# Optimization experiments

Measured on AMD Instinct MI355X. Metric: run time of the kernel, lower is better.

## Reference

```python
import jax, jax.numpy as jnp
import numpy as np

B, N = 4, 4096
CIN, COUT = 64, 64
K, R, BOX = 3, 32, 4
MLP = COUT * 4
HEADS = 4
EPS = 0.0


def setup_inputs() -> dict:
    key = jax.random.key(0)
    ks = jax.random.split(key, 16)
    s = lambda i, shape: jax.random.normal(ks[i], shape, jnp.float32) * 0.05
    return dict(
        features=jax.random.normal(ks[0], (B, CIN, N), jnp.float32),
        coords=jax.random.normal(ks[1], (B, 3, N), jnp.float32),
        conv_w=s(2, (COUT, CIN, K, K, K)), conv_b=jnp.zeros((COUT,), jnp.float32),
        ln1_g=jnp.ones((COUT,), jnp.float32), ln1_b=jnp.zeros((COUT,), jnp.float32),
        qkv_w=s(3, (3 * COUT, COUT)), qkv_b=jnp.zeros((3 * COUT,), jnp.float32),
        proj_w=s(4, (COUT, COUT)), proj_b=jnp.zeros((COUT,), jnp.float32),
        ln2_g=jnp.ones((COUT,), jnp.float32), ln2_b=jnp.zeros((COUT,), jnp.float32),
        mlp_w1=s(5, (MLP, COUT)), mlp_b1=jnp.zeros((MLP,), jnp.float32),
        mlp_w2=s(6, (COUT, MLP)), mlp_b2=jnp.zeros((COUT,), jnp.float32),
        se_w1=s(7, (COUT // 8, COUT)), se_w2=s(8, (COUT, COUT // 8)),
        pt_in_w=s(9, (COUT, CIN)), pt_in_b=jnp.zeros((COUT,), jnp.float32),
        q_w=s(10, (COUT // 4, COUT)), k_w=s(11, (COUT // 4, COUT)),
        v_w=s(12, (COUT, COUT)),
        trans_w=s(13, (COUT, COUT)), trans_b=jnp.zeros((COUT,), jnp.float32),
    )


def layernorm(x, g, b):
    m = x.mean(-1, keepdims=True)
    v = x.var(-1, keepdims=True)
    return (x - m) * jax.lax.rsqrt(v + 1e-5) * g + b


def voxelize(features, coords):
    # PVCNN-style: center, normalize to [0,1], scale to [0, R-1]; scatter-mean.
    c = coords - coords.mean(axis=2, keepdims=True)  # (B,3,N)
    mx = jnp.sqrt((c ** 2).sum(axis=1, keepdims=True)).max(axis=2, keepdims=True)
    nc = c / (2.0 * mx + EPS) + 0.5
    nc = jnp.clip(nc * R, 0.0, R - 1)  # float coords in [0, R-1]
    vc = jnp.round(nc).astype(jnp.int32)
    idx = (vc[:, 0] * R + vc[:, 1]) * R + vc[:, 2]
    idx = (idx + jnp.arange(B, dtype=jnp.int32)[:, None] * R ** 3).reshape(-1)
    flat = features.transpose(0, 2, 1).reshape(B * N, CIN)
    sums = jax.ops.segment_sum(flat, idx, num_segments=B * R ** 3)
    cnt = jax.ops.segment_sum(jnp.ones((B * N,), jnp.float32), idx, num_segments=B * R ** 3)
    avg = sums / jnp.maximum(cnt, 1.0)[:, None]
    grid = avg.reshape(B, R, R, R, CIN).transpose(0, 4, 1, 2, 3)  # (B,C,R,R,R)
    return grid, nc


def devoxelize(grid, nc):
    # trilinear gather from (B,C,R,R,R) at float coords nc (B,3,N)
    g = grid.reshape(B, COUT, R ** 3)
    x0 = jnp.floor(nc)
    f = nc - x0
    x0 = x0.astype(jnp.int32)
    out = jnp.zeros((B, COUT, N), jnp.float32)
    for dx in (0, 1):
        for dy in (0, 1):
            for dz in (0, 1):
                xi = jnp.clip(x0[:, 0] + dx, 0, R - 1)
                yi = jnp.clip(x0[:, 1] + dy, 0, R - 1)
                zi = jnp.clip(x0[:, 2] + dz, 0, R - 1)
                idx = (xi * R + yi) * R + zi  # (B,N)
                w = ((f[:, 0] if dx else 1 - f[:, 0]) *
                     (f[:, 1] if dy else 1 - f[:, 1]) *
                     (f[:, 2] if dz else 1 - f[:, 2]))
                vals = jnp.take_along_axis(g, jnp.broadcast_to(idx[:, None, :], (B, COUT, N)), axis=2)
                out = out + vals * w[:, None, :]
    return out


def voxel_encoder(grid, conv_w, conv_b, ln1_g, ln1_b, qkv_w, qkv_b, proj_w, proj_b,
                  ln2_g, ln2_b, mlp_w1, mlp_b1, mlp_w2, mlp_b2):
    x = jax.lax.conv_general_dilated(grid, conv_w, (1, 1, 1), 'SAME',
                                     dimension_numbers=('NCDHW', 'OIDHW', 'NCDHW'))
    x = jax.nn.relu(x + conv_b[None, :, None, None, None])
    nb = R // BOX
    # window partition -> (B*nb^3, BOX^3, C)
    t = x.transpose(0, 2, 3, 4, 1).reshape(B, nb, BOX, nb, BOX, nb, BOX, COUT)
    t = t.transpose(0, 1, 3, 5, 2, 4, 6, 7).reshape(B * nb ** 3, BOX ** 3, COUT)
    h = layernorm(t, ln1_g, ln1_b)
    qkv = h @ qkv_w.T + qkv_b
    q, k, v = jnp.split(qkv, 3, axis=-1)
    hd = COUT // HEADS
    sh = lambda z: z.reshape(z.shape[0], z.shape[1], HEADS, hd).transpose(0, 2, 1, 3)
    q, k, v = sh(q), sh(k), sh(v)
    attn = jax.nn.softmax(jnp.einsum('whid,whjd->whij', q, k) / np.float32(np.sqrt(hd)), axis=-1)
    o = jnp.einsum('whij,whjd->whid', attn, v).transpose(0, 2, 1, 3).reshape(t.shape)
    t = t + (o @ proj_w.T + proj_b)
    h = layernorm(t, ln2_g, ln2_b)
    t = t + (jax.nn.gelu(h @ mlp_w1.T + mlp_b1) @ mlp_w2.T + mlp_b2)
    t = t.reshape(B, nb, nb, nb, BOX, BOX, BOX, COUT)
    t = t.transpose(0, 1, 4, 2, 5, 3, 6, 7).reshape(B, R, R, R, COUT)
    return t.transpose(0, 4, 1, 2, 3)


def se3d(x, w1, w2):
    s = x.mean(axis=(2, 3, 4))  # (B,C)
    s = jax.nn.sigmoid(jax.nn.relu(s @ w1.T) @ w2.T)
    return x * s[:, :, None, None, None]


def point_branch(features, pt_in_w, pt_in_b, q_w, k_w, v_w, trans_w, trans_b):
    # PCT-style offset self-attention over points (shared transformer)
    x = jax.nn.relu(jnp.einsum('oc,bcn->bon', pt_in_w, features) + pt_in_b[None, :, None])
    q = jnp.einsum('dc,bcn->bdn', q_w, x)
    k = jnp.einsum('dc,bcn->bdn', k_w, x)
    v = jnp.einsum('oc,bcn->bon', v_w, x)
    attn = jax.nn.softmax(jnp.einsum('bdn,bdm->bnm', q, k) / np.float32(np.sqrt(q.shape[1])), axis=-1)
    o = jnp.einsum('bom,bnm->bon', v, attn)
    off = jax.nn.relu(jnp.einsum('oc,bcn->bon', trans_w, x - o) + trans_b[None, :, None])
    return x + off


def reference(features, coords, conv_w, conv_b, ln1_g, ln1_b, qkv_w, qkv_b, proj_w, proj_b,
              ln2_g, ln2_b, mlp_w1, mlp_b1, mlp_w2, mlp_b2, se_w1, se_w2,
              pt_in_w, pt_in_b, q_w, k_w, v_w, trans_w, trans_b):
    grid, nc = voxelize(features, coords)
    vf = voxel_encoder(grid, conv_w, conv_b, ln1_g, ln1_b, qkv_w, qkv_b, proj_w, proj_b,
                       ln2_g, ln2_b, mlp_w1, mlp_b1, mlp_w2, mlp_b2)
    vf = se3d(vf, se_w1, se_w2)
    vf = devoxelize(vf, nc)
    fused = vf + point_branch(features, pt_in_w, pt_in_b, q_w, k_w, v_w, trans_w, trans_b)
    return fused, coords
```

## Files before the change

kernel.cpp:

```cpp
#include <hip/hip_runtime.h>

#define BN 4
#define NP 4096
#define RV 32
#define VX (RV*RV*RV)

typedef __attribute__((ext_vector_type(8))) short bf16x8;
typedef __attribute__((ext_vector_type(4))) float f32x4;

__device__ __forceinline__ float bf2f(unsigned short u){
  union{unsigned u;float f;}v; v.u=((unsigned)u)<<16; return v.f; }
__device__ __forceinline__ unsigned short f2bf(float f){
  union{float f;unsigned u;}v; v.f=f; unsigned r=v.u + 0x7fffu + ((v.u>>16)&1u);
  return (unsigned short)(r>>16); }
__device__ __forceinline__ float2 bfp2f2(unsigned p){
  union{unsigned u;float f;}a,b; a.u=p<<16; b.u=p&0xffff0000u;
  float2 r; r.x=a.f; r.y=b.f; return r; }
__device__ __forceinline__ unsigned pack2bf(float a, float b){
  return (unsigned)f2bf(a) | ((unsigned)f2bf(b) << 16); }

union ABu { uint4 u; bf16x8 v; };

__global__ void stats_kernel(const float* __restrict__ coords, float* __restrict__ stats)
{
  __shared__ float red[256];
  __shared__ float mean[3];
  const int b = blockIdx.x;
  const int tid = threadIdx.x;
  float s0=0.f,s1=0.f,s2=0.f;
  for (int n = tid; n < NP; n += 256) {
    s0 += coords[((size_t)(b*3)+0)*NP + n];
    s1 += coords[((size_t)(b*3)+1)*NP + n];
    s2 += coords[((size_t)(b*3)+2)*NP + n];
  }
  float sv[3] = {s0,s1,s2};
  for (int ax = 0; ax < 3; ax++) {
    __syncthreads();
    red[tid] = sv[ax];
    __syncthreads();
    for (int st = 128; st > 0; st >>= 1) {
      if (tid < st) red[tid] += red[tid + st];
      __syncthreads();
    }
    if (tid == 0) mean[ax] = red[0] * (1.f / NP);
  }
  __syncthreads();
  float mx = 0.f;
  for (int n = tid; n < NP; n += 256) {
    float d0 = coords[((size_t)(b*3)+0)*NP + n] - mean[0];
    float d1 = coords[((size_t)(b*3)+1)*NP + n] - mean[1];
    float d2 = coords[((size_t)(b*3)+2)*NP + n] - mean[2];
    mx = fmaxf(mx, sqrtf(d0*d0 + d1*d1 + d2*d2));
  }
  __syncthreads();
  red[tid] = mx;
  __syncthreads();
  for (int st = 128; st > 0; st >>= 1) {
    if (tid < st) red[tid] = fmaxf(red[tid], red[tid + st]);
    __syncthreads();
  }
  if (tid == 0) {
    stats[b*4+0] = mean[0]; stats[b*4+1] = mean[1];
    stats[b*4+2] = mean[2]; stats[b*4+3] = red[0];
  }
}

__global__ __launch_bounds__(256) void scatter_kernel(
    const float* __restrict__ features, const float* __restrict__ coords,
    const float* __restrict__ stats, float* __restrict__ nc,
    float* __restrict__ sums, float* __restrict__ cnt)
{
  __shared__ float f_s[64*65];
  const int tid = threadIdx.x;
  const int blk = blockIdx.x;
  const int b = blk >> 6;
  const int n0 = (blk & 63) * 64;
  for (int e = tid; e < 4096; e += 256) {
    int c = e >> 6, nl = e & 63;
    f_s[nl*65 + c] = features[((size_t)(b*64 + c))*NP + n0 + nl];
  }
  const int part = tid & 3, nl = tid >> 2;
  const int n = n0 + nl;
  float m0 = stats[b*4+0], m1 = stats[b*4+1], m2 = stats[b*4+2], mx = stats[b*4+3];
  float inv = 1.f / (2.f * mx);
  float c0 = (coords[((size_t)(b*3)+0)*NP + n] - m0) * inv + 0.5f;
  float c1 = (coords[((size_t)(b*3)+1)*NP + n] - m1) * inv + 0.5f;
  float c2 = (coords[((size_t)(b*3)+2)*NP + n] - m2) * inv + 0.5f;
  float g0 = fminf(fmaxf(c0 * 32.f, 0.f), 31.f);
  float g1 = fminf(fmaxf(c1 * 32.f, 0.f), 31.f);
  float g2 = fminf(fmaxf(c2 * 32.f, 0.f), 31.f);
  int v0 = (int)rintf(g0), v1 = (int)rintf(g1), v2 = (int)rintf(g2);
  int idx = (v0*32 + v1)*32 + v2 + b*VX;
  if (part == 0) {
    nc[((size_t)(b*3)+0)*NP + n] = g0;
    nc[((size_t)(b*3)+1)*NP + n] = g1;
    nc[((size_t)(b*3)+2)*NP + n] = g2;
    atomicAdd(&cnt[idx], 1.f);
  }
  __syncthreads();
  float* sp = sums + (size_t)idx*64;
  #pragma unroll
  for (int j = 0; j < 16; j++) {
    int i = part*16 + j;
    atomicAdd(&sp[i], f_s[nl*65 + i]);
  }
}

__global__ void wprep_kernel(const float* __restrict__ wt, unsigned short* __restrict__ wpre)
{
  int t = blockIdx.x*256 + threadIdx.x;
  if (t >= 27*64*8) return;
  int c16 = t & 7, o = (t >> 3) & 63, tap = t >> 9;
  size_t dst = ((size_t)(tap*64 + o)*8 + (c16 ^ (o & 7))) * 8;
  #pragma unroll
  for (int j = 0; j < 8; j++) {
    int i = c16*8 + j;
    wpre[dst + j] = f2bf(wt[(o*64 + i)*27 + tap]);
  }
}

__global__ void eprep_kernel(const float* __restrict__ qkv_w, const float* __restrict__ proj_w,
                             const float* __restrict__ w1, const float* __restrict__ w2,
                             const float* __restrict__ pt_in_w, const float* __restrict__ q_w,
                             const float* __restrict__ k_w, const float* __restrict__ v_w,
                             unsigned short* __restrict__ dst)
{
  int t = blockIdx.x*256 + threadIdx.x;
  if (t >= 59392) return;
  float v;
  if (t < 4096)       v = qkv_w[t] * 0.25f;
  else if (t < 12288) v = qkv_w[t];
  else if (t < 16384) v = proj_w[t-12288];
  else if (t < 32768) v = w1[t-16384];
  else if (t < 49152) v = w2[t-32768];
  else {
    int t2 = t - 49152;
    if (t2 < 4096)      v = pt_in_w[t2];
    else if (t2 < 5120) v = q_w[t2-4096] * 0.25f;
    else if (t2 < 6144) v = k_w[t2-5120];
    else                v = v_w[t2-6144];
  }
  dst[t] = f2bf(v);
}

__global__ __launch_bounds__(256) void conv_mfma_kernel(
    const float* __restrict__ sums, const float* __restrict__ cnt,
    const unsigned short* __restrict__ wpre,
    const float* __restrict__ bias, unsigned short* __restrict__ gout)
{
  __shared__ uint4 plane[6*34*8];
  __shared__ uint4 wsm[3*64*8];
  const int tid = threadIdx.x;
  const int blk = blockIdx.x;
  const int yq = blk & 7, z = (blk >> 3) & 31, b = blk >> 8;
  const int y0 = yq * 4;
  const int w  = tid >> 6;
  const int lm = tid & 15;
  const int kg = (tid >> 4) & 3;

  f32x4 acc[2][4];
  #pragma unroll
  for (int mt = 0; mt < 2; mt++)
    #pragma unroll
    for (int nt = 0; nt < 4; nt++)
      #pragma unroll
      for (int r = 0; r < 4; r++) acc[mt][nt][r] = 0.f;

  float bv[4];
  #pragma unroll
  for (int nt = 0; nt < 4; nt++) bv[nt] = bias[nt*16 + lm];

  for (int kd = 0; kd < 3; kd++) {
    const int zz = z + kd - 1;
    if (zz < 0 || zz >= 32) continue;
    __syncthreads();
    for (int e = tid; e < 6*34*8; e += 256) {
      int c16 = e & 7;
      int sx  = (e >> 3) % 34;
      int yl  = e / (34*8);
      int yy = y0 - 1 + yl, x = sx - 1;
      uint4 val = make_uint4(0u,0u,0u,0u);
      if (yy >= 0 && yy < 32 && x >= 0 && x < 32) {
        size_t vox = (size_t)(b*VX) + (zz*32 + yy)*32 + x;
        float rc = 1.f / fmaxf(cnt[vox], 1.f);
        const float* src = sums + vox*64 + c16*8;
        float4 f0 = *(const float4*)(src);
        float4 f1 = *(const float4*)(src + 4);
        val.x = pack2bf(f0.x*rc, f0.y*rc);
        val.y = pack2bf(f0.z*rc, f0.w*rc);
        val.z = pack2bf(f1.x*rc, f1.y*rc);
        val.w = pack2bf(f1.z*rc, f1.w*rc);
      }
      plane[(yl*34 + sx)*8 + (c16 ^ (sx & 7))] = val;
    }
    for (int kh = 0; kh < 3; kh++) {
      __syncthreads();
      const uint4* wsrc = (const uint4*)wpre + (size_t)((kd*3 + kh)*3)*512;
      for (int e = tid; e < 1536; e += 256) wsm[e] = wsrc[e];
      __syncthreads();
      const int yi = w + kh;
      #pragma unroll
      for (int kw = 0; kw < 3; kw++) {
        const int sxa = lm + kw, sxb = sxa + 16;
        const int swz = sxa & 7;
        #pragma unroll
        for (int ch = 0; ch < 2; ch++) {
          const int cb = ch*4 + kg;
          ABu a0, a1, w0, w1, w2, w3;
          a0.u = plane[(yi*34 + sxa)*8 + (cb ^ swz)];
          a1.u = plane[(yi*34 + sxb)*8 + (cb ^ swz)];
          const int wsz = cb ^ (lm & 7);
          w0.u = wsm[(kw*64 +      lm)*8 + wsz];
          w1.u = wsm[(kw*64 + 16 + lm)*8 + wsz];
          w2.u = wsm[(kw*64 + 32 + lm)*8 + wsz];
          w3.u = wsm[(kw*64 + 48 + lm)*8 + wsz];
          acc[0][0] = __builtin_amdgcn_mfma_f32_16x16x32_bf16(a0.v, w0.v, acc[0][0], 0,0,0);
          acc[1][0] = __builtin_amdgcn_mfma_f32_16x16x32_bf16(a1.v, w0.v, acc[1][0], 0,0,0);
          acc[0][1] = __builtin_amdgcn_mfma_f32_16x16x32_bf16(a0.v, w1.v, acc[0][1], 0,0,0);
          acc[1][1] = __builtin_amdgcn_mfma_f32_16x16x32_bf16(a1.v, w1.v, acc[1][1], 0,0,0);
          acc[0][2] = __builtin_amdgcn_mfma_f32_16x16x32_bf16(a0.v, w2.v, acc[0][2], 0,0,0);
          acc[1][2] = __builtin_amdgcn_mfma_f32_16x16x32_bf16(a1.v, w2.v, acc[1][2], 0,0,0);
          acc[0][3] = __builtin_amdgcn_mfma_f32_16x16x32_bf16(a0.v, w3.v, acc[0][3], 0,0,0);
          acc[1][3] = __builtin_amdgcn_mfma_f32_16x16x32_bf16(a1.v, w3.v, acc[1][3], 0,0,0);
        }
      }
    }
  }
  const int y = y0 + w;
  #pragma unroll
  for (int mt = 0; mt < 2; mt++) {
    #pragma unroll
    for (int r = 0; r < 4; r++) {
      const int x = mt*16 + kg*4 + r;
      unsigned short* dst = gout + ((size_t)(b*VX) + (z*32 + y)*32 + x)*64 + lm;
      #pragma unroll
      for (int nt = 0; nt < 4; nt++)
        dst[nt*16] = f2bf(fmaxf(acc[mt][nt][r] + bv[nt], 0.f));
    }
  }
}

__global__ __launch_bounds__(256) void encoder_kernel(
    unsigned short* __restrict__ grid,
    const float* __restrict__ ln1_g, const float* __restrict__ ln1_b,
    const float* __restrict__ qkv_b, const float* __restrict__ proj_b,
    const float* __restrict__ ln2_g, const float* __restrict__ ln2_b,
    const float* __restrict__ b1, const float* __restrict__ b2,
    const unsigned short* __restrict__ encw,
    float* __restrict__ se_sum)
{
  __shared__ unsigned short t_b[64*72];
  __shared__ unsigned short h_b[64*72];
  __shared__ unsigned short q_b[64*72];
  __shared__ unsigned short k_b[64*72];
  __shared__ unsigned short v_b[64*72];
  __shared__ float mean_s[64], rstd_s[64];
  __shared__ float sered[256];

  const unsigned short* wqb = encw;
  const unsigned short* wpb = encw + 12288;
  const unsigned short* w1b = encw + 16384;
  const unsigned short* w2b = encw + 32768;

  const int tid = threadIdx.x;
  const int w = tid >> 6;
  const int lane = tid & 63;
  const int cl = lane & 15;
  const int quad = lane >> 4;
  const int win = blockIdx.x;
  const int b = win >> 9, wn = win & 511;
  const int zb = wn >> 6, yb = (wn >> 3) & 7, xb = wn & 7;
  const size_t gb = (size_t)b * VX * 64;

  for (int e = tid; e < 1024; e += 256) {
    int tok = e >> 4, cg = e & 15;
    int zl = tok >> 4, yl = (tok >> 2) & 3, xl = tok & 3;
    int vox = ((zb*4+zl)*32 + (yb*4+yl))*32 + (xb*4+xl);
    *(uint2*)(t_b + tok*72 + cg*4) = *(const uint2*)(grid + gb + (size_t)vox*64 + cg*4);
  }
  __syncthreads();
  {
    int i = tid >> 2, part = tid & 3;
    float sum = 0.f, sq = 0.f;
    for (int c = part; c < 64; c += 4) { float x = bf2f(t_b[i*72+c]); sum += x; sq += x*x; }
    sum += __shfl_xor(sum, 1); sq += __shfl_xor(sq, 1);
    sum += __shfl_xor(sum, 2); sq += __shfl_xor(sq, 2);
    if (part == 0) {
      float m = sum * (1.f/64.f);
      float var = sq * (1.f/64.f) - m*m;
      mean_s[i] = m; rstd_s[i] = rsqrtf(var + 1e-5f);
    }
  }
  __syncthreads();
  for (int e = tid; e < 4096; e += 256) {
    int tok = e >> 6, c = e & 63;
    float h = (bf2f(t_b[tok*72+c]) - mean_s[tok]) * rstd_s[tok] * ln1_g[c] + ln1_b[c];
    h_b[tok*72 + c] = f2bf(h);
  }
  __syncthreads();
  {
    #pragma unroll
    for (int ci = 0; ci < 3; ci++) {
      const int d0 = 48*w + ci*16;
      ABu a0, a1;
      a0.u = *(const uint4*)(wqb + (d0 + cl)*64 + quad*8);
      a1.u = *(const uint4*)(wqb + (d0 + cl)*64 + 32 + quad*8);
      float4 bias4 = *(const float4*)(qkv_b + d0 + quad*4);
      if (d0 < 64) { bias4.x *= 0.25f; bias4.y *= 0.25f; bias4.z *= 0.25f; bias4.w *= 0.25f; }
      #pragma unroll
      for (int tt = 0; tt < 4; tt++) {
        ABu h0, h1;
        h0.u = *(const uint4*)(h_b + (tt*16 + cl)*72 + quad*8);
        h1.u = *(const uint4*)(h_b + (tt*16 + cl)*72 + 32 + quad*8);
        f32x4 d = {0.f,0.f,0.f,0.f};
        d = __builtin_amdgcn_mfma_f32_16x16x32_bf16(a0.v, h0.v, d, 0,0,0);
        d = __builtin_amdgcn_mfma_f32_16x16x32_bf16(a1.v, h1.v, d, 0,0,0);
        if (d0 < 64) {
          *(uint2*)(q_b + (tt*16+cl)*72 + d0 + quad*4) =
            make_uint2(pack2bf(d[0]+bias4.x, d[1]+bias4.y),
                       pack2bf(d[2]+bias4.z, d[3]+bias4.w));
        } else if (d0 < 128) {
          *(uint2*)(k_b + (tt*16+cl)*72 + (d0-64) + quad*4) =
            make_uint2(pack2bf(d[0]+bias4.x, d[1]+bias4.y),
                       pack2bf(d[2]+bias4.z, d[3]+bias4.w));
        } else {
          const float* bp = (const float*)&bias4;
          #pragma unroll
          for (int r = 0; r < 4; r++)
            v_b[((d0-128) + quad*4 + r)*72 + tt*16 + cl] = f2bf(d[r] + bp[r]);
        }
      }
    }
  }
  __syncthreads();
  uint2 pk[4];
  {
    const uint4 z4 = make_uint4(0u,0u,0u,0u);
    #pragma unroll
    for (int h = 0; h < 4; h++) {
      const int hb = h*16;
      ABu bq;
      if (quad < 2) bq.u = *(const uint4*)(q_b + (w*16 + cl)*72 + hb + quad*8);
      else bq.u = z4;
      float sc[4][4];
      #pragma unroll
      for (int tj = 0; tj < 4; tj++) {
        ABu ak;
        if (quad < 2) ak.u = *(const uint4*)(k_b + (tj*16 + cl)*72 + hb + quad*8);
        else ak.u = z4;
        f32x4 d = {0.f,0.f,0.f,0.f};
        d = __builtin_amdgcn_mfma_f32_16x16x32_bf16(ak.v, bq.v, d, 0,0,0);
        #pragma unroll
        for (int r = 0; r < 4; r++) sc[tj][r] = d[r];
      }
      float mx = -1e30f;
      #pragma unroll
      for (int tj = 0; tj < 4; tj++)
        #pragma unroll
        for (int r = 0; r < 4; r++) mx = fmaxf(mx, sc[tj][r]);
      mx = fmaxf(mx, __shfl_xor(mx, 16));
      mx = fmaxf(mx, __shfl_xor(mx, 32));
      float psum = 0.f;
      #pragma unroll
      for (int tj = 0; tj < 4; tj++) {
        float p0 = __expf(sc[tj][0]-mx), p1 = __expf(sc[tj][1]-mx);
        float p2 = __expf(sc[tj][2]-mx), p3 = __expf(sc[tj][3]-mx);
        psum += p0+p1+p2+p3;
        *(uint2*)(h_b + (w*16+cl)*72 + tj*16 + quad*4) =
            make_uint2(pack2bf(p0,p1), pack2bf(p2,p3));
      }
      psum += __shfl_xor(psum, 16);
      psum += __shfl_xor(psum, 32);
      float inv = 1.f / psum;
      f32x4 oacc = {0.f,0.f,0.f,0.f};
      #pragma unroll
      for (int kk = 0; kk < 2; kk++) {
        ABu av, bp;
        av.u = *(const uint4*)(v_b + (hb + cl)*72 + kk*32 + quad*8);
        bp.u = *(const uint4*)(h_b + (w*16 + cl)*72 + kk*32 + quad*8);
        oacc = __builtin_amdgcn_mfma_f32_16x16x32_bf16(av.v, bp.v, oacc, 0,0,0);
      }
      pk[h] = make_uint2(pack2bf(oacc[0]*inv, oacc[1]*inv),
                         pack2bf(oacc[2]*inv, oacc[3]*inv));
    }
  }
  __syncthreads();
  #pragma unroll
  for (int h = 0; h < 4; h++)
    *(uint2*)(k_b + (w*16+cl)*72 + h*16 + quad*4) = pk[h];
  __syncthreads();
  {
    const int c0 = w*16;
    ABu a0, a1;
    a0.u = *(const uint4*)(wpb + (c0 + cl)*64 + quad*8);
    a1.u = *(const uint4*)(wpb + (c0 + cl)*64 + 32 + quad*8);
    float4 pb4 = *(const float4*)(proj_b + c0 + quad*4);
    #pragma unroll
    for (int tt = 0; tt < 4; tt++) {
      ABu o0, o1;
      o0.u = *(const uint4*)(k_b + (tt*16 + cl)*72 + quad*8);
      o1.u = *(const uint4*)(k_b + (tt*16 + cl)*72 + 32 + quad*8);
      f32x4 d = {0.f,0.f,0.f,0.f};
      d = __builtin_amdgcn_mfma_f32_16x16x32_bf16(a0.v, o0.v, d, 0,0,0);
      d = __builtin_amdgcn_mfma_f32_16x16x32_bf16(a1.v, o1.v, d, 0,0,0);
      uint2* tp = (uint2*)(t_b + (tt*16+cl)*72 + c0 + quad*4);
      uint2 told = *tp;
      float2 t01 = bfp2f2(told.x), t23 = bfp2f2(told.y);
      *tp = make_uint2(pack2bf(t01.x + d[0] + pb4.x, t01.y + d[1] + pb4.y),
                       pack2bf(t23.x + d[2] + pb4.z, t23.y + d[3] + pb4.w));
    }
  }
  __syncthreads();
  {
    int i = tid >> 2, part = tid & 3;
    float sum = 0.f, sq = 0.f;
    for (int c = part; c < 64; c += 4) { float x = bf2f(t_b[i*72+c]); sum += x; sq += x*x; }
    sum += __shfl_xor(sum, 1); sq += __shfl_xor(sq, 1);
    sum += __shfl_xor(sum, 2); sq += __shfl_xor(sq, 2);
    if (part == 0) {
      float m = sum * (1.f/64.f);
      float var = sq * (1.f/64.f) - m*m;
      mean_s[i] = m; rstd_s[i] = rsqrtf(var + 1e-5f);
    }
  }
  __syncthreads();
  for (int e = tid; e < 4096; e += 256) {
    int tok = e >> 6, c = e & 63;
    float h = (bf2f(t_b[tok*72+c]) - mean_s[tok]) * rstd_s[tok] * ln2_g[c] + ln2_b[c];
    h_b[tok*72 + c] = f2bf(h);
  }
  __syncthreads();
  {
    const int c0 = w*16;
    ABu hb0[4], hb1[4];
    #pragma unroll
    for (int tt = 0; tt < 4; tt++) {
      hb0[tt].u = *(const uint4*)(h_b + (tt*16 + cl)*72 + quad*8);
      hb1[tt].u = *(const uint4*)(h_b + (tt*16 + cl)*72 + 32 + quad*8);
    }
    f32x4 acc2[4];
    #pragma unroll
    for (int tt = 0; tt < 4; tt++)
      #pragma unroll
      for (int r = 0; r < 4; r++) acc2[tt][r] = 0.f;
    for (int ch = 0; ch < 4; ch++) {
      const int m0 = ch*64 + w*16;
      ABu a0, a1;
      a0.u = *(const uint4*)(w1b + (m0 + cl)*64 + quad*8);
      a1.u = *(const uint4*)(w1b + (m0 + cl)*64 + 32 + quad*8);
      float4 b14 = *(const float4*)(b1 + m0 + quad*4);
      const float* bp = (const float*)&b14;
      #pragma unroll
      for (int tt = 0; tt < 4; tt++) {
        f32x4 d = {0.f,0.f,0.f,0.f};
        d = __builtin_amdgcn_mfma_f32_16x16x32_bf16(a0.v, hb0[tt].v, d, 0,0,0);
        d = __builtin_amdgcn_mfma_f32_16x16x32_bf16(a1.v, hb1[tt].v, d, 0,0,0);
        float g[4];
        #pragma unroll
        for (int r = 0; r < 4; r++) {
          float x = d[r] + bp[r];
          float u = 1.5957691f * (x + 0.044715f*x*x*x);
          g[r] = x / (1.f + __expf(-u));
        }
        *(uint2*)(q_b + (tt*16+cl)*72 + w*16 + quad*4) =
            make_uint2(pack2bf(g[0],g[1]), pack2bf(g[2],g[3]));
      }
      __syncthreads();
      ABu a20, a21;
      a20.u = *(const uint4*)(w2b + (c0 + cl)*256 + ch*64 + quad*8);
      a21.u = *(const uint4*)(w2b + (c0 + cl)*256 + ch*64 + 32 + quad*8);
      #pragma unroll
      for (int tt = 0; tt < 4; tt++) {
        ABu bh0, bh1;
        bh0.u = *(const uint4*)(q_b + (tt*16 + cl)*72 + quad*8);
        bh1.u = *(const uint4*)(q_b + (tt*16 + cl)*72 + 32 + quad*8);
        acc2[tt] = __builtin_amdgcn_mfma_f32_16x16x32_bf16(a20.v, bh0.v, acc2[tt], 0,0,0);
        acc2[tt] = __builtin_amdgcn_mfma_f32_16x16x32_bf16(a21.v, bh1.v, acc2[tt], 0,0,0);
      }
      __syncthreads();
    }
    float4 b24 = *(const float4*)(b2 + c0 + quad*4);
    #pragma unroll
    for (int tt = 0; tt < 4; tt++) {
      uint2* tp = (uint2*)(t_b + (tt*16+cl)*72 + c0 + quad*4);
      uint2 told = *tp;
      float2 t01 = bfp2f2(told.x), t23 = bfp2f2(told.y);
      *tp = make_uint2(pack2bf(t01.x + acc2[tt][0] + b24.x, t01.y + acc2[tt][1] + b24.y),
                       pack2bf(t23.x + acc2[tt][2] + b24.z, t23.y + acc2[tt][3] + b24.w));
    }
  }
  __syncthreads();
  for (int e = tid; e < 1024; e += 256) {
    int tok = e >> 4, cg = e & 15;
    int zl = tok >> 4, yl = (tok >> 2) & 3, xl = tok & 3;
    int vox = ((zb*4+zl)*32 + (yb*4+yl))*32 + (xb*4+xl);
    *(uint2*)(grid + gb + (size_t)vox*64 + cg*4) = *(const uint2*)(t_b + tok*72 + cg*4);
  }
  {
    int c = tid & 63, quarter = tid >> 6;
    float ps = 0.f;
    #pragma unroll
    for (int t = 0; t < 16; t++) ps += bf2f(t_b[(quarter*16+t)*72 + c]);
    sered[quarter*64 + c] = ps;
  }
  __syncthreads();
  if (tid < 64)
    atomicAdd(&se_sum[b*64 + tid],
              sered[tid] + sered[64+tid] + sered[128+tid] + sered[192+tid]);
}

__global__ void se_kernel(const float* __restrict__ se_sum, const float* __restrict__ w1,
                          const float* __restrict__ w2, float* __restrict__ scale)
{
  __shared__ float mean_s[256];
  __shared__ float z1[32];
  int tid = threadIdx.x;
  mean_s[tid] = se_sum[tid] * (1.f / VX);
  __syncthreads();
  if (tid < 32) {
    int bb = tid >> 3, j = tid & 7;
    float a = 0.f;
    for (int c = 0; c < 64; c++) a += mean_s[bb*64 + c] * w1[j*64 + c];
    z1[tid] = fmaxf(a, 0.f);
  }
  __syncthreads();
  int b = tid >> 6, c = tid & 63;
  float a = 0.f;
  for (int j = 0; j < 8; j++) a += z1[b*8 + j] * w2[c*8 + j];
  scale[tid] = 1.f / (1.f + __expf(-a));
}

__global__ __launch_bounds__(256) void point_in_kernel(
    const float* __restrict__ features, const float* __restrict__ pt_in_b,
    const unsigned short* __restrict__ ptw,
    float* __restrict__ x_t, unsigned short* __restrict__ q_bf,
    unsigned short* __restrict__ k_bf, unsigned short* __restrict__ v_tt)
{
  __shared__ unsigned short f_b[64*72];
  __shared__ unsigned short x_b[64*72];
  const int tid = threadIdx.x;
  const int blk = blockIdx.x;
  const int b = blk >> 6;
  const int n0 = (blk & 63) * 64;
  const int w = tid >> 6;
  const int lane = tid & 63;
  const int cl = lane & 15;
  const int quad = lane >> 4;

  for (int e = tid; e < 4096; e += 256) {
    int c = e >> 6, nl = e & 63;
    f_b[nl*72 + c] = f2bf(features[((size_t)(b*64 + c))*NP + n0 + nl]);
  }
  __syncthreads();
  const int m0 = w*16;
  {
    ABu a0, a1;
    a0.u = *(const uint4*)(ptw + (m0 + cl)*64 + quad*8);
    a1.u = *(const uint4*)(ptw + (m0 + cl)*64 + 32 + quad*8);
    float4 bi = *(const float4*)(pt_in_b + m0 + quad*4);
    #pragma unroll
    for (int tt = 0; tt < 4; tt++) {
      ABu f0, f1;
      f0.u = *(const uint4*)(f_b + (tt*16 + cl)*72 + quad*8);
      f1.u = *(const uint4*)(f_b + (tt*16 + cl)*72 + 32 + quad*8);
      f32x4 d = {0.f,0.f,0.f,0.f};
      d = __builtin_amdgcn_mfma_f32_16x16x32_bf16(a0.v, f0.v, d, 0,0,0);
      d = __builtin_amdgcn_mfma_f32_16x16x32_bf16(a1.v, f1.v, d, 0,0,0);
      float x0 = fmaxf(d[0]+bi.x, 0.f), x1 = fmaxf(d[1]+bi.y, 0.f);
      float x2 = fmaxf(d[2]+bi.z, 0.f), x3 = fmaxf(d[3]+bi.w, 0.f);
      const int n = tt*16 + cl;
      *(float4*)&x_t[((size_t)(b*NP) + n0 + n)*64 + m0 + quad*4] =
          make_float4(x0, x1, x2, x3);
      *(uint2*)(x_b + n*72 + m0 + quad*4) = make_uint2(pack2bf(x0,x1), pack2bf(x2,x3));
    }
  }
  __syncthreads();
  {
    const unsigned short* vwb = ptw + 6144;
    ABu a0, a1;
    a0.u = *(const uint4*)(vwb + (m0 + cl)*64 + quad*8);
    a1.u = *(const uint4*)(vwb + (m0 + cl)*64 + 32 + quad*8);
    #pragma unroll
    for (int tt = 0; tt < 4; tt++) {
      ABu x0, x1;
      x0.u = *(const uint4*)(x_b + (tt*16 + cl)*72 + quad*8);
      x1.u = *(const uint4*)(x_b + (tt*16 + cl)*72 + 32 + quad*8);
      f32x4 d = {0.f,0.f,0.f,0.f};
      d = __builtin_amdgcn_mfma_f32_16x16x32_bf16(a0.v, x0.v, d, 0,0,0);
      d = __builtin_amdgcn_mfma_f32_16x16x32_bf16(a1.v, x1.v, d, 0,0,0);
      const int n = n0 + tt*16 + cl;
      #pragma unroll
      for (int r = 0; r < 4; r++)
        v_tt[((size_t)(b*64) + m0 + quad*4 + r)*NP + n] = f2bf(d[r]);
    }
  }
  {
    const int which = w & 1, half = w >> 1;
    const unsigned short* wp = ptw + (which ? 5120 : 4096);
    unsigned short* dst = which ? k_bf : q_bf;
    ABu a0, a1;
    a0.u = *(const uint4*)(wp + cl*64 + quad*8);
    a1.u = *(const uint4*)(wp + cl*64 + 32 + quad*8);
    #pragma unroll
    for (int th = 0; th < 2; th++) {
      const int tt = half*2 + th;
      ABu x0, x1;
      x0.u = *(const uint4*)(x_b + (tt*16 + cl)*72 + quad*8);
      x1.u = *(const uint4*)(x_b + (tt*16 + cl)*72 + 32 + quad*8);
      f32x4 d = {0.f,0.f,0.f,0.f};
      d = __builtin_amdgcn_mfma_f32_16x16x32_bf16(a0.v, x0.v, d, 0,0,0);
      d = __builtin_amdgcn_mfma_f32_16x16x32_bf16(a1.v, x1.v, d, 0,0,0);
      const int n = tt*16 + cl;
      *(uint2*)(dst + ((size_t)(b*NP) + n0 + n)*16 + quad*4) =
          make_uint2(pack2bf(d[0],d[1]), pack2bf(d[2],d[3]));
    }
  }
}

__global__ __launch_bounds__(256) void point_attn_kernel(
    const unsigned short* __restrict__ q_bf, const unsigned short* __restrict__ k_bf,
    const unsigned short* __restrict__ v_tt,
    float* __restrict__ opart, float2* __restrict__ mlbuf)
{
  __shared__ unsigned short q_s[64*24];
  __shared__ unsigned short k_sh[2][64*24];
  __shared__ unsigned short v_sh[2][64*72];
  __shared__ unsigned short p_s[64*72];
  const int tid = threadIdx.x;
  const int blk = blockIdx.x;
  const int b = blk >> 8;
  const int nb = (blk >> 2) & 63;
  const int s = blk & 3;
  const int n0 = nb * 64;
  const int t_beg = s*16, t_end = s*16 + 16;
  const int w = tid >> 6;
  const int lane = tid & 63;
  const int cl = lane & 15;
  const int quad = lane >> 4;
  const uint4 z4 = make_uint4(0u,0u,0u,0u);

  const unsigned* qbu = (const unsigned*)q_bf;
  const unsigned* kbu = (const unsigned*)k_bf;
  const unsigned* vtu = (const unsigned*)v_tt;
  unsigned* q_su = (unsigned*)q_s;

  {
    unsigned* kd = (unsigned*)k_sh[0];
    unsigned* vd = (unsigned*)v_sh[0];
    for (int e = tid; e < 512; e += 256) {
      int tok = e >> 3, du = e & 7;
      q_su[tok*12 + du] = qbu[((size_t)(b*NP) + n0 + tok)*8 + du];
      kd[tok*12 + du]   = kbu[((size_t)(b*NP) + t_beg*64 + tok)*8 + du];
    }
    for (int e = tid; e < 2048; e += 256) {
      int cc = e >> 5, tu = e & 31;
      vd[cc*36 + tu] = vtu[((size_t)(b*64) + cc)*2048 + t_beg*32 + tu];
    }
  }
  float m_run = -1e30f, l_run = 0.f;
  f32x4 acc[4];
  #pragma unroll
  for (int ct = 0; ct < 4; ct++)
    #pragma unroll
    for (int r = 0; r < 4; r++) acc[ct][r] = 0.f;
  __syncthreads();

  ABu bq;
  if (quad < 2) bq.u = *(const uint4*)(q_s + (w*16 + cl)*24 + quad*8);
  else bq.u = z4;

  for (int t = t_beg; t < t_end; t++) {
    const int cur = t & 1;
    unsigned pk[2], pv[8];
    if (t+1 < t_end) {
      const int m1 = (t+1)*64;
      #pragma unroll
      for (int i = 0; i < 2; i++) {
        int e = tid + i*256;
        pk[i] = kbu[((size_t)(b*NP) + m1 + (e>>3))*8 + (e&7)];
      }
      #pragma unroll
      for (int i = 0; i < 8; i++) {
        int e = tid + i*256;
        pv[i] = vtu[((size_t)(b*64) + (e>>5))*2048 + (m1>>1) + (e&31)];
      }
    }
    const unsigned short* ks = k_sh[cur];
    const unsigned short* vs = v_sh[cur];
    float sc[4][4];
    #pragma unroll
    for (int tj = 0; tj < 4; tj++) {
      ABu ak;
      if (quad < 2) ak.u = *(const uint4*)(ks + (tj*16 + cl)*24 + quad*8);
      else ak.u = z4;
      f32x4 d = {0.f,0.f,0.f,0.f};
      d = __builtin_amdgcn_mfma_f32_16x16x32_bf16(ak.v, bq.v, d, 0,0,0);
      #pragma unroll
      for (int r = 0; r < 4; r++) sc[tj][r] = d[r];
    }
    float tmax = -1e30f;
    #pragma unroll
    for (int tj = 0; tj < 4; tj++)
      #pragma unroll
      for (int r = 0; r < 4; r++) tmax = fmaxf(tmax, sc[tj][r]);
    tmax = fmaxf(tmax, __shfl_xor(tmax, 16));
    tmax = fmaxf(tmax, __shfl_xor(tmax, 32));
    float mnew = fmaxf(m_run, tmax);
    float alpha = __expf(m_run - mnew);
    float psum = 0.f;
    #pragma unroll
    for (int tj = 0; tj < 4; tj++) {
      float p0 = __expf(sc[tj][0]-mnew), p1 = __expf(sc[tj][1]-mnew);
      float p2 = __expf(sc[tj][2]-mnew), p3 = __expf(sc[tj][3]-mnew);
      psum += p0+p1+p2+p3;
      *(uint2*)(p_s + (w*16+cl)*72 + tj*16 + quad*4) =
          make_uint2(pack2bf(p0,p1), pack2bf(p2,p3));
    }
    psum += __shfl_xor(psum, 16);
    psum += __shfl_xor(psum, 32);
    l_run = l_run*alpha + psum;
    m_run = mnew;
    #pragma unroll
    for (int ct = 0; ct < 4; ct++)
      #pragma unroll
      for (int r = 0; r < 4; r++) acc[ct][r] *= alpha;
    #pragma unroll
    for (int kk = 0; kk < 2; kk++) {
      ABu bp;
      bp.u = *(const uint4*)(p_s + (w*16 + cl)*72 + kk*32 + quad*8);
      #pragma unroll
      for (int ct = 0; ct < 4; ct++) {
        ABu av;
        av.u = *(const uint4*)(vs + (ct*16 + cl)*72 + kk*32 + quad*8);
        acc[ct] = __builtin_amdgcn_mfma_f32_16x16x32_bf16(av.v, bp.v, acc[ct], 0,0,0);
      }
    }
    __syncthreads();
    if (t+1 < t_end) {
      unsigned* kd = (unsigned*)k_sh[1-cur];
      unsigned* vd = (unsigned*)v_sh[1-cur];
      #pragma unroll
      for (int i = 0; i < 2; i++) {
        int e = tid + i*256;
        kd[(e>>3)*12 + (e&7)] = pk[i];
      }
      #pragma unroll
      for (int i = 0; i < 8; i++) {
        int e = tid + i*256;
        vd[(e>>5)*36 + (e&31)] = pv[i];
      }
    }
    __syncthreads();
  }
  const int tok = n0 + w*16 + cl;
  #pragma unroll
  for (int ct = 0; ct < 4; ct++) {
    float4 o4;
    o4.x = acc[ct][0]; o4.y = acc[ct][1]; o4.z = acc[ct][2]; o4.w = acc[ct][3];
    *(float4*)&opart[(((size_t)(s*BN + b))*NP + tok)*64 + ct*16 + quad*4] = o4;
  }
  if (quad == 0)
    mlbuf[(size_t)(s*BN + b)*NP + tok] = make_float2(m_run, l_run);
}

__global__ __launch_bounds__(256) void fuse_kernel(
    const float* __restrict__ x_t, const float* __restrict__ opart,
    const float2* __restrict__ mlbuf,
    const float* __restrict__ trans_w, const float* __restrict__ trans_b,
    const unsigned short* __restrict__ grid, const float* __restrict__ se_scale,
    const float* __restrict__ nc, float* __restrict__ out)
{
  __shared__ float tw_s[64*65];
  __shared__ float d_s[32*65];
  __shared__ float r_s[64*33];
  __shared__ float mw[32][6];
  const int tid = threadIdx.x;
  const int blk = blockIdx.x;
  const int b = blk >> 7;
  const int n0 = (blk & 127) * 32;
  for (int e = tid; e < 4096; e += 256) {
    int c = e >> 6, k = e & 63;
    tw_s[c*65 + k] = trans_w[e];
  }
  if (tid < 32) {
    int nl = tid;
    float m[4], l[4];
    #pragma unroll
    for (int s = 0; s < 4; s++) {
      float2 v = mlbuf[(size_t)(s*BN + b)*NP + n0 + nl];
      m[s] = v.x; l[s] = v.y;
    }
    float M = fmaxf(fmaxf(m[0], m[1]), fmaxf(m[2], m[3]));
    float L = 0.f;
    #pragma unroll
    for (int s = 0; s < 4; s++) {
      float ws = __expf(m[s] - M);
      mw[nl][s] = ws;
      L += l[s] * ws;
    }
    mw[nl][4] = 1.f / L;
  }
  __syncthreads();
  for (int e = tid; e < 2048; e += 256) {
    int nl = e >> 6, c = e & 63;
    size_t pbase = ((size_t)(b*NP) + n0 + nl)*64 + c;
    const size_t sstr = (size_t)BN*NP*64;
    float o = opart[pbase]        * mw[nl][0] + opart[pbase +   sstr] * mw[nl][1]
            + opart[pbase+2*sstr] * mw[nl][2] + opart[pbase + 3*sstr] * mw[nl][3];
    o *= mw[nl][4];
    d_s[nl*65 + c] = x_t[pbase] - o;
  }
  __syncthreads();
  const int cl = tid & 63, g = tid >> 6;
  const float ses = se_scale[b*64 + cl];
  const float tb = trans_b[cl];
  for (int t = 0; t < 8; t++) {
    int nl = g*8 + t;
    int n = n0 + nl;
    float off = 0.f;
    for (int k = 0; k < 64; k++) off += tw_s[cl*65 + k] * d_s[nl*65 + k];
    off = fmaxf(off + tb, 0.f);
    float ncx = nc[((size_t)(b*3)+0)*NP + n];
    float ncy = nc[((size_t)(b*3)+1)*NP + n];
    float ncz = nc[((size_t)(b*3)+2)*NP + n];
    float fx0 = floorf(ncx), fy0 = floorf(ncy), fz0 = floorf(ncz);
    int x0 = (int)fx0, y0 = (int)fy0, z0 = (int)fz0;
    float fx = ncx - fx0, fy = ncy - fy0, fz = ncz - fz0;
    float wx[2] = {1.f-fx, fx}, wy[2] = {1.f-fy, fy}, wz[2] = {1.f-fz, fz};
    float vf = 0.f;
    #pragma unroll
    for (int cor = 0; cor < 8; cor++) {
      int dx = cor >> 2, dy = (cor >> 1) & 1, dz = cor & 1;
      int xi = min(x0+dx, 31), yi = min(y0+dy, 31), zi = min(z0+dz, 31);
      float wgt = wx[dx]*wy[dy]*wz[dz];
      vf += wgt * bf2f(grid[((size_t)(b*VX) + (xi*32+yi)*32 + zi)*64 + cl]);
    }
    vf *= ses;
    float xval = x_t[((size_t)(b*NP) + n)*64 + cl];
    r_s[cl*33 + nl] = xval + off + vf;
  }
  __syncthreads();
  for (int e = tid; e < 2048; e += 256) {
    int c = e >> 5, nl = e & 31;
    out[((size_t)(b*64) + c)*NP + n0 + nl] = r_s[c*33 + nl];
  }
}

extern "C" void kernel_launch(void* const* d_in, const int* in_sizes, int n_in,
                              void* d_out, int out_size, void* d_ws, size_t ws_size,
                              hipStream_t stream)
{
  const float* features = (const float*)d_in[0];
  const float* coords   = (const float*)d_in[1];
  const float* conv_w   = (const float*)d_in[2];
  const float* conv_b   = (const float*)d_in[3];
  const float* ln1_g    = (const float*)d_in[4];
  const float* ln1_b    = (const float*)d_in[5];
  const float* qkv_w    = (const float*)d_in[6];
  const float* qkv_b    = (const float*)d_in[7];
  const float* proj_w   = (const float*)d_in[8];
  const float* proj_b   = (const float*)d_in[9];
  const float* ln2_g    = (const float*)d_in[10];
  const float* ln2_b    = (const float*)d_in[11];
  const float* mlp_w1   = (const float*)d_in[12];
  const float* mlp_b1   = (const float*)d_in[13];
  const float* mlp_w2   = (const float*)d_in[14];
  const float* mlp_b2   = (const float*)d_in[15];
  const float* se_w1    = (const float*)d_in[16];
  const float* se_w2    = (const float*)d_in[17];
  const float* pt_in_w  = (const float*)d_in[18];
  const float* pt_in_b  = (const float*)d_in[19];
  const float* q_w      = (const float*)d_in[20];
  const float* k_w      = (const float*)d_in[21];
  const float* v_w      = (const float*)d_in[22];
  const float* v_trans_w= (const float*)d_in[23];
  const float* v_trans_b= (const float*)d_in[24];

  char* ws = (char*)d_ws;
  float* stats    = (float*)(ws + 0);
  float* se_sum   = (float*)(ws + 256);
  float* se_scale = (float*)(ws + 1280);
  float* nc       = (float*)(ws + 4096);
  float* cnt      = (float*)(ws + 200704);
  float* grid0    = (float*)(ws + 724992);
  unsigned short* grid1b = (unsigned short*)(ws + 34279424);
  float* x_t = (float*)(ws + 724992);
  unsigned short* q_bf = (unsigned short*)(ws + 724992 + 4194304);
  unsigned short* k_bf = (unsigned short*)(ws + 724992 + 5242880);
  unsigned short* v_tt = (unsigned short*)(ws + 724992 + 6291456);
  float*  opart = (float*)(ws + 724992 + 10485760);
  float2* mlbuf = (float2*)(ws + 724992 + 27787264);
  unsigned short* wpre = (unsigned short*)d_out;
  unsigned short* encw = (unsigned short*)((char*)d_out + 221184);

  hipMemsetAsync(se_sum, 0, 1024, stream);
  hipMemsetAsync(cnt, 0, 524288 + 33554432, stream);

  wprep_kernel<<<54, 256, 0, stream>>>(conv_w, wpre);
  eprep_kernel<<<232, 256, 0, stream>>>(qkv_w, proj_w, mlp_w1, mlp_w2,
      pt_in_w, q_w, k_w, v_w, encw);
  stats_kernel<<<BN, 256, 0, stream>>>(coords, stats);
  scatter_kernel<<<256, 256, 0, stream>>>(features, coords, stats, nc, grid0, cnt);
  conv_mfma_kernel<<<1024, 256, 0, stream>>>(grid0, cnt, wpre, conv_b, grid1b);
  encoder_kernel<<<2048, 256, 0, stream>>>(grid1b, ln1_g, ln1_b, qkv_b, proj_b,
      ln2_g, ln2_b, mlp_b1, mlp_b2, encw, se_sum);
  se_kernel<<<1, 256, 0, stream>>>(se_sum, se_w1, se_w2, se_scale);
  point_in_kernel<<<256, 256, 0, stream>>>(features, pt_in_b, encw + 49152,
      x_t, q_bf, k_bf, v_tt);
  point_attn_kernel<<<1024, 256, 0, stream>>>(q_bf, k_bf, v_tt, opart, mlbuf);
  fuse_kernel<<<512, 256, 0, stream>>>(x_t, opart, mlbuf, v_trans_w, v_trans_b,
      grid1b, se_scale, nc, (float*)d_out);
  hipMemcpyAsync((char*)d_out + (size_t)BN*64*NP*4, coords, (size_t)BN*3*NP*4,
                 hipMemcpyDeviceToDevice, stream);
}
```

Measured before the change: 413.0 us.

## Repartition QKV projection by token and merge LDS buffers to cut shared memory

Result: no change. 415.9 us (+0.7%).

```diff
diff --git a/kernel.cpp b/kernel.cpp
--- a/kernel.cpp
+++ b/kernel.cpp
@@ -250,8 +250,7 @@
     float* __restrict__ se_sum)
 {
   __shared__ unsigned short t_b[64*72];
-  __shared__ unsigned short h_b[64*72];
-  __shared__ unsigned short q_b[64*72];
+  __shared__ unsigned short a_b[64*72];
   __shared__ unsigned short k_b[64*72];
   __shared__ unsigned short v_b[64*72];
   __shared__ float mean_s[64], rstd_s[64];
@@ -295,40 +294,37 @@
   for (int e = tid; e < 4096; e += 256) {
     int tok = e >> 6, c = e & 63;
     float h = (bf2f(t_b[tok*72+c]) - mean_s[tok]) * rstd_s[tok] * ln1_g[c] + ln1_b[c];
-    h_b[tok*72 + c] = f2bf(h);
-  }
-  __syncthreads();
-  {
-    #pragma unroll
-    for (int ci = 0; ci < 3; ci++) {
-      const int d0 = 48*w + ci*16;
+    a_b[tok*72 + c] = f2bf(h);
+  }
+  __syncthreads();
+  {
+    ABu hB0, hB1;
+    hB0.u = *(const uint4*)(a_b + (w*16 + cl)*72 + quad*8);
+    hB1.u = *(const uint4*)(a_b + (w*16 + cl)*72 + 32 + quad*8);
+    #pragma unroll
+    for (int mt = 0; mt < 12; mt++) {
+      const int d0 = mt*16;
       ABu a0, a1;
       a0.u = *(const uint4*)(wqb + (d0 + cl)*64 + quad*8);
       a1.u = *(const uint4*)(wqb + (d0 + cl)*64 + 32 + quad*8);
       float4 bias4 = *(const float4*)(qkv_b + d0 + quad*4);
-      if (d0 < 64) { bias4.x *= 0.25f; bias4.y *= 0.25f; bias4.z *= 0.25f; bias4.w *= 0.25f; }
-      #pragma unroll
-      for (int tt = 0; tt < 4; tt++) {
-        ABu h0, h1;
-        h0.u = *(const uint4*)(h_b + (tt*16 + cl)*72 + quad*8);
-        h1.u = *(const uint4*)(h_b + (tt*16 + cl)*72 + 32 + quad*8);
-        f32x4 d = {0.f,0.f,0.f,0.f};
-        d = __builtin_amdgcn_mfma_f32_16x16x32_bf16(a0.v, h0.v, d, 0,0,0);
-        d = __builtin_amdgcn_mfma_f32_16x16x32_bf16(a1.v, h1.v, d, 0,0,0);
-        if (d0 < 64) {
-          *(uint2*)(q_b + (tt*16+cl)*72 + d0 + quad*4) =
-            make_uint2(pack2bf(d[0]+bias4.x, d[1]+bias4.y),
-                       pack2bf(d[2]+bias4.z, d[3]+bias4.w));
-        } else if (d0 < 128) {
-          *(uint2*)(k_b + (tt*16+cl)*72 + (d0-64) + quad*4) =
-            make_uint2(pack2bf(d[0]+bias4.x, d[1]+bias4.y),
-                       pack2bf(d[2]+bias4.z, d[3]+bias4.w));
-        } else {
-          const float* bp = (const float*)&bias4;
-          #pragma unroll
-          for (int r = 0; r < 4; r++)
-            v_b[((d0-128) + quad*4 + r)*72 + tt*16 + cl] = f2bf(d[r] + bp[r]);
-        }
+      if (mt < 4) { bias4.x *= 0.25f; bias4.y *= 0.25f; bias4.z *= 0.25f; bias4.w *= 0.25f; }
+      f32x4 d = {0.f,0.f,0.f,0.f};
+      d = __builtin_amdgcn_mfma_f32_16x16x32_bf16(a0.v, hB0.v, d, 0,0,0);
+      d = __builtin_amdgcn_mfma_f32_16x16x32_bf16(a1.v, hB1.v, d, 0,0,0);
+      if (mt < 4) {
+        *(uint2*)(a_b + (w*16+cl)*72 + d0 + quad*4) =
+          make_uint2(pack2bf(d[0]+bias4.x, d[1]+bias4.y),
+                     pack2bf(d[2]+bias4.z, d[3]+bias4.w));
+      } else if (mt < 8) {
+        *(uint2*)(k_b + (w*16+cl)*72 + (d0-64) + quad*4) =
+          make_uint2(pack2bf(d[0]+bias4.x, d[1]+bias4.y),
+                     pack2bf(d[2]+bias4.z, d[3]+bias4.w));
+      } else {
+        const float* bp = (const float*)&bias4;
+        #pragma unroll
+        for (int r = 0; r < 4; r++)
+          v_b[((d0-128) + quad*4 + r)*72 + w*16 + cl] = f2bf(d[r] + bp[r]);
       }
     }
   }
@@ -336,12 +332,15 @@
   uint2 pk[4];
   {
     const uint4 z4 = make_uint4(0u,0u,0u,0u);
+    ABu bqr[4];
+    #pragma unroll
+    for (int h = 0; h < 4; h++) {
+      if (quad < 2) bqr[h].u = *(const uint4*)(a_b + (w*16 + cl)*72 + h*16 + quad*8);
+      else bqr[h].u = z4;
+    }
     #pragma unroll
     for (int h = 0; h < 4; h++) {
       const int hb = h*16;
-      ABu bq;
-      if (quad < 2) bq.u = *(const uint4*)(q_b + (w*16 + cl)*72 + hb + quad*8);
-      else bq.u = z4;
       float sc[4][4];
       #pragma unroll
       for (int tj = 0; tj < 4; tj++) {
@@ -349,7 +348,7 @@
         if (quad < 2) ak.u = *(const uint4*)(k_b + (tj*16 + cl)*72 + hb + quad*8);
         else ak.u = z4;
         f32x4 d = {0.f,0.f,0.f,0.f};
-        d = __builtin_amdgcn_mfma_f32_16x16x32_bf16(ak.v, bq.v, d, 0,0,0);
+        d = __builtin_amdgcn_mfma_f32_16x16x32_bf16(ak.v, bqr[h].v, d, 0,0,0);
         #pragma unroll
         for (int r = 0; r < 4; r++) sc[tj][r] = d[r];
       }
@@ -366,7 +365,7 @@
         float p0 = __expf(sc[tj][0]-mx), p1 = __expf(sc[tj][1]-mx);
         float p2 = __expf(sc[tj][2]-mx), p3 = __expf(sc[tj][3]-mx);
         psum += p0+p1+p2+p3;
-        *(uint2*)(h_b + (w*16+cl)*72 + tj*16 + quad*4) =
+        *(uint2*)(a_b + (w*16+cl)*72 + tj*16 + quad*4) =
             make_uint2(pack2bf(p0,p1), pack2bf(p2,p3));
       }
       psum += __shfl_xor(psum, 16);
@@ -377,7 +376,7 @@
       for (int kk = 0; kk < 2; kk++) {
         ABu av, bp;
         av.u = *(const uint4*)(v_b + (hb + cl)*72 + kk*32 + quad*8);
-        bp.u = *(const uint4*)(h_b + (w*16 + cl)*72 + kk*32 + quad*8);
+        bp.u = *(const uint4*)(a_b + (w*16 + cl)*72 + kk*32 + quad*8);
         oacc = __builtin_amdgcn_mfma_f32_16x16x32_bf16(av.v, bp.v, oacc, 0,0,0);
       }
       pk[h] = make_uint2(pack2bf(oacc[0]*inv, oacc[1]*inv),
@@ -427,7 +426,7 @@
   for (int e = tid; e < 4096; e += 256) {
     int tok = e >> 6, c = e & 63;
     float h = (bf2f(t_b[tok*72+c]) - mean_s[tok]) * rstd_s[tok] * ln2_g[c] + ln2_b[c];
-    h_b[tok*72 + c] = f2bf(h);
+    a_b[tok*72 + c] = f2bf(h);
   }
   __syncthreads();
   {
@@ -435,8 +434,8 @@
     ABu hb0[4], hb1[4];
     #pragma unroll
     for (int tt = 0; tt < 4; tt++) {
-      hb0[tt].u = *(const uint4*)(h_b + (tt*16 + cl)*72 + quad*8);
-      hb1[tt].u = *(const uint4*)(h_b + (tt*16 + cl)*72 + 32 + quad*8);
+      hb0[tt].u = *(const uint4*)(a_b + (tt*16 + cl)*72 + quad*8);
+      hb1[tt].u = *(const uint4*)(a_b + (tt*16 + cl)*72 + 32 + quad*8);
     }
     f32x4 acc2[4];
     #pragma unroll
@@ -462,7 +461,7 @@
           float u = 1.5957691f * (x + 0.044715f*x*x*x);
           g[r] = x / (1.f + __expf(-u));
         }
-        *(uint2*)(q_b + (tt*16+cl)*72 + w*16 + quad*4) =
+        *(uint2*)(k_b + (tt*16+cl)*72 + w*16 + quad*4) =
             make_uint2(pack2bf(g[0],g[1]), pack2bf(g[2],g[3]));
       }
       __syncthreads();
@@ -472,8 +471,8 @@
       #pragma unroll
       for (int tt = 0; tt < 4; tt++) {
         ABu bh0, bh1;
-        bh0.u = *(const uint4*)(q_b + (tt*16 + cl)*72 + quad*8);
-        bh1.u = *(const uint4*)(q_b + (tt*16 + cl)*72 + 32 + quad*8);
+        bh0.u = *(const uint4*)(k_b + (tt*16 + cl)*72 + quad*8);
+        bh1.u = *(const uint4*)(k_b + (tt*16 + cl)*72 + 32 + quad*8);
         acc2[tt] = __builtin_amdgcn_mfma_f32_16x16x32_bf16(a20.v, bh0.v, acc2[tt], 0,0,0);
         acc2[tt] = __builtin_amdgcn_mfma_f32_16x16x32_bf16(a21.v, bh1.v, acc2[tt], 0,0,0);
       }
```
